# Optimization experiments

Measured on AMD Instinct MI355X. Metric: run time of the kernel, lower is better.

The kernel has to match this reference:

```python
import jax, jax.numpy as jnp
import numpy as np

N_HEAD = 16


def setup_inputs() -> dict:
    key = jax.random.key(0)
    ks = jax.random.split(key, 6)
    B, T, H = 4, 2048, 1024
    inp = jax.random.normal(ks[0], (B, T, H), dtype=jnp.float32)
    # padding mask: valid prefix of random length in [T//2, T] per batch row
    lengths = jax.random.randint(ks[1], (B, 1), T // 2, T + 1)
    mask = jnp.arange(T)[None, :] < lengths  # (B, T) bool
    s = 0.02
    w_qkv = jax.random.normal(ks[2], (H, 3 * H), dtype=jnp.float32) * s
    b_qkv = jax.random.normal(ks[3], (3 * H,), dtype=jnp.float32) * s
    w_out = jax.random.normal(ks[4], (H, H), dtype=jnp.float32) * s
    b_out = jax.random.normal(ks[5], (H,), dtype=jnp.float32) * s
    return {"input": inp, "mask": mask, "w_qkv": w_qkv, "b_qkv": b_qkv,
            "w_out": w_out, "b_out": b_out}


def reference(input, mask, w_qkv, b_qkv, w_out, b_out):
    B, T, H = input.shape
    hd = H // N_HEAD
    qkv = input @ w_qkv + b_qkv                       # (B, T, 3H)
    q, k, v = jnp.split(qkv, 3, axis=-1)
    # (B, T, H) -> (B, nh, T, hd)
    q = q.reshape(B, T, N_HEAD, hd).transpose(0, 2, 1, 3)
    k = k.reshape(B, T, N_HEAD, hd).transpose(0, 2, 1, 3)
    v = v.reshape(B, T, N_HEAD, hd).transpose(0, 2, 1, 3)
    scores = jnp.einsum('bhqd,bhkd->bhqk', q, k) / jnp.sqrt(jnp.float32(hd))
    causal = jnp.tril(jnp.ones((T, T), dtype=bool))   # (T, T)
    full_mask = causal[None, None, :, :] & mask[:, None, None, :]  # (B,1,T,T) bcast over heads
    scores = jnp.where(full_mask, scores, -jnp.inf)
    attn = jax.nn.softmax(scores, axis=-1)            # (B, nh, T, T)
    o = jnp.einsum('bhqk,bhkd->bhqd', attn, v)        # (B, nh, T, hd)
    o = o.transpose(0, 2, 1, 3).reshape(B, T, H)
    return o @ w_out + b_out
```

## Files before the change

### kernel.cpp

```cpp
#include <hip/hip_runtime.h>
#include <math.h>

#define B_  4
#define T_  2048
#define H_  1024
#define NH  16
#define HD  64
#define H3  3072

typedef short bf16x8 __attribute__((ext_vector_type(8)));
typedef short bf16x4 __attribute__((ext_vector_type(4)));
typedef float f32x4  __attribute__((ext_vector_type(4)));

#define SC2F 0.18033688011112042f

__device__ __forceinline__ unsigned short f2bf(float f) {
    union { float f; unsigned u; } v; v.f = f;
    unsigned u = v.u;
    unsigned r = (u + 0x7fffu + ((u >> 16) & 1u)) >> 16;
    return (unsigned short)r;
}

__device__ __forceinline__ void gload_lds16(const void* g, void* l) {
    __builtin_amdgcn_global_load_lds(
        (const __attribute__((address_space(1))) unsigned*)g,
        (__attribute__((address_space(3))) unsigned*)l, 16, 0, 0);
}

__device__ __forceinline__ f32x4 mfma_16x16x16_bf16(bf16x4 a, bf16x4 b, f32x4 c) {
#if __has_builtin(__builtin_amdgcn_mfma_f32_16x16x16_bf16)
    return __builtin_amdgcn_mfma_f32_16x16x16_bf16(a, b, c, 0, 0, 0);
#elif __has_builtin(__builtin_amdgcn_mfma_f32_16x16x16bf16_1k)
    return __builtin_amdgcn_mfma_f32_16x16x16bf16_1k(a, b, c, 0, 0, 0);
#else
    f32x4 d;
    asm volatile("v_mfma_f32_16x16x16_bf16 %0, %1, %2, %3"
                 : "=v"(d) : "v"(a), "v"(b), "v"(c));
    return d;
#endif
}

__global__ void lengths_kernel(const void* mask, int* lengths) {
    int b = blockIdx.x;
    int t = threadIdx.x;
    const unsigned* mu = (const unsigned*)mask;
    bool is_byte = (mu[0] == 0x01010101u);
    int cnt = 0;
    if (is_byte) {
        const unsigned char* m8 = (const unsigned char*)mask;
        for (int i = t; i < T_; i += 256) cnt += (m8[b * T_ + i] != 0);
    } else {
        const unsigned* m32 = (const unsigned*)mask;
        for (int i = t; i < T_; i += 256) cnt += (m32[b * T_ + i] != 0);
    }
    __shared__ int red[256];
    red[t] = cnt;
    __syncthreads();
    for (int s = 128; s > 0; s >>= 1) {
        if (t < s) red[t] += red[t + s];
        __syncthreads();
    }
    if (t == 0) lengths[b] = red[0];
}

__global__ void convert_bf16_kernel(const float* __restrict__ x,
                                    unsigned short* __restrict__ y, int n) {
    int i = (blockIdx.x * 256 + threadIdx.x) * 4;
    if (i < n) {
        float4 v = *(const float4*)(x + i);
        ushort4 o;
        o.x = f2bf(v.x); o.y = f2bf(v.y); o.z = f2bf(v.z); o.w = f2bf(v.w);
        *(ushort4*)(y + i) = o;
    }
}

__global__ void transpose_bf16_kernel(const float* __restrict__ in,
                                      unsigned short* __restrict__ out,
                                      int K, int N) {
    __shared__ unsigned short tile[32][33];
    int kb = blockIdx.y * 32, nb = blockIdx.x * 32;
    int tx = threadIdx.x, ty = threadIdx.y;
    for (int i = 0; i < 32; i += 8)
        tile[ty + i][tx] = f2bf(in[(long)(kb + ty + i) * N + nb + tx]);
    __syncthreads();
    for (int i = 0; i < 32; i += 8)
        out[(long)(nb + ty + i) * K + kb + tx] = tile[tx][ty + i];
}

template <bool BF16_OUT, bool KSCALE, bool VSPLIT>
__global__ __launch_bounds__(256) void gemm_kernel(
    const unsigned short* __restrict__ A,
    const unsigned short* __restrict__ Bt,
    const float* __restrict__ bias,
    void* __restrict__ C,
    unsigned short* __restrict__ Vt,
    int M, int N, int K)
{
    __shared__ unsigned short Asm[128][32];
    __shared__ unsigned short Bsm[128][32];

    int tn = blockIdx.x * 128, tm = blockIdx.y * 128;
    int tid = threadIdx.x;
    int wid = tid >> 6, lane = tid & 63, quad = lane >> 4, lr = lane & 15;
    int wm = (wid & 1) * 64, wn = (wid >> 1) * 64;
    int grow = lane >> 2, gcol = (lane & 3) * 8;

    f32x4 acc[4][4] = {};

    for (int k0 = 0; k0 < K; k0 += 32) {
        __syncthreads();
#pragma unroll
        for (int t = 0; t < 2; t++) {
            int ar = wid * 32 + t * 16 + grow;
            gload_lds16(A  + (long)(tm + ar) * K + k0 + gcol, &Asm[wid * 32 + t * 16][0]);
            gload_lds16(Bt + (long)(tn + ar) * K + k0 + gcol, &Bsm[wid * 32 + t * 16][0]);
        }
        __syncthreads();

        bf16x8 af[4], bfv[4];
#pragma unroll
        for (int i = 0; i < 4; i++) af[i]  = *(const bf16x8*)(&Asm[wm + i * 16 + lr][quad * 8]);
#pragma unroll
        for (int j = 0; j < 4; j++) bfv[j] = *(const bf16x8*)(&Bsm[wn + j * 16 + lr][quad * 8]);
#pragma unroll
        for (int i = 0; i < 4; i++)
#pragma unroll
            for (int j = 0; j < 4; j++)
                acc[i][j] = __builtin_amdgcn_mfma_f32_16x16x32_bf16(af[i], bfv[j], acc[i][j], 0, 0, 0);
    }

    if (VSPLIT && tn >= 2 * H_) {
#pragma unroll
        for (int i = 0; i < 4; i++)
#pragma unroll
            for (int j = 0; j < 4; j++) {
                int col = tn + wn + j * 16 + lr;
                float bs = bias[col];
                int feat = col - 2 * H_;
                int tok0 = tm + wm + i * 16 + quad * 4;
                int bb = tok0 >> 11;
                unsigned d0 = (unsigned)f2bf(acc[i][j][0] + bs) |
                              ((unsigned)f2bf(acc[i][j][1] + bs) << 16);
                unsigned d1 = (unsigned)f2bf(acc[i][j][2] + bs) |
                              ((unsigned)f2bf(acc[i][j][3] + bs) << 16);
                unsigned short* dst = Vt + ((long)(bb * 1024 + feat)) * T_ + (tok0 & (T_ - 1));
                *(uint2*)dst = make_uint2(d0, d1);
            }
        return;
    }

#pragma unroll
    for (int i = 0; i < 4; i++)
#pragma unroll
        for (int j = 0; j < 4; j++) {
            int col = tn + wn + j * 16 + lr;
            float bs = bias[col];
            bool ks = KSCALE && (col >= H_) && (col < 2 * H_);
#pragma unroll
            for (int r = 0; r < 4; r++) {
                int row = tm + wm + i * 16 + quad * 4 + r;
                float v = acc[i][j][r] + bs;
                if (ks) v *= SC2F;
                if (BF16_OUT)
                    ((unsigned short*)C)[(long)row * N + col] = f2bf(v);
                else
                    ((float*)C)[(long)row * N + col] = v;
            }
        }
}

__global__ __launch_bounds__(256) void attn_kernel(
    const unsigned short* __restrict__ QKV,
    const unsigned short* __restrict__ Vt,
    const int* __restrict__ lengths,
    unsigned short* __restrict__ O)
{
    int idx = blockIdx.x;
    int bh = idx & 63;
    int pr = idx >> 6;
    int b = bh >> 4, h = bh & 15;
    int len = lengths[b];

    int tid = threadIdx.x;
    int wid = tid >> 6, lane = tid & 63, quad = lane >> 4, lr = lane & 15;

    __shared__ unsigned short Qs[128][72];
    __shared__ unsigned short Kd[2][64][72];
    __shared__ unsigned short Vd[2][64][72];

    const long qkv_base = (long)b * T_ * H3;
    int srow = tid >> 2, scb = (tid & 3) * 16;
    const unsigned short* kbase = QKV + qkv_base + (long)srow * H3 + H_ + h * HD + scb;
    const unsigned short* vbase = Vt + ((long)(bh * 64 + srow)) * T_ + scb;

    for (int pass = 0; pass < 2; pass++) {
        int qt = pass ? pr : (15 - pr);
        int q0 = qt * 128;

        __syncthreads();
        {
            int row = tid >> 1, cb = (tid & 1) * 32;
            const unsigned short* src = QKV + qkv_base + (long)(q0 + row) * H3 + h * HD + cb;
#pragma unroll
            for (int i = 0; i < 4; i++)
                *(float4*)(&Qs[row][cb + i * 8]) = *(const float4*)(src + i * 8);
        }
        {
            float4 k0 = *(const float4*)(kbase);
            float4 k1 = *(const float4*)(kbase + 8);
            float4 v0 = *(const float4*)(vbase);
            float4 v1 = *(const float4*)(vbase + 8);
            *(float4*)(&Kd[0][srow][scb])     = k0;
            *(float4*)(&Kd[0][srow][scb + 8]) = k1;
            *(float4*)(&Vd[0][srow][scb])     = v0;
            *(float4*)(&Vd[0][srow][scb + 8]) = v1;
        }
        __syncthreads();

        bf16x8 qf[2][2];
#pragma unroll
        for (int nq = 0; nq < 2; nq++)
#pragma unroll
            for (int ks = 0; ks < 2; ks++)
                qf[nq][ks] = *(const bf16x8*)(&Qs[wid * 32 + nq * 16 + lr][ks * 32 + quad * 8]);

        float l_i[2] = { 0.f, 0.f };
        f32x4 Oacc[4][2] = {};

        int kmax = min(q0 + 127, len - 1);
        int n_kt = (kmax >> 6) + 1;
        int q_wave_lo = q0 + wid * 32;
        int q_wave_hi = q_wave_lo + 31;
        int myq[2] = { q_wave_lo + lr, q_wave_lo + 16 + lr };

        const unsigned short* kp = kbase + (long)64 * H3;
        const unsigned short* vp = vbase + 64;

        for (int kt = 0; kt < n_kt; kt++) {
            int cur = kt & 1;
            float4 pk0, pk1, pv0, pv1;
            bool pf = (kt + 1 < n_kt);
            if (pf) {
                pk0 = *(const float4*)(kp);
                pk1 = *(const float4*)(kp + 8);
                pv0 = *(const float4*)(vp);
                pv1 = *(const float4*)(vp + 8);
                kp += (long)64 * H3;
                vp += 64;
            }

            int k_lo = kt * 64;
            if (!(k_lo > q_wave_hi || k_lo >= len)) {
                f32x4 Sacc[4][2] = {};
#pragma unroll
                for (int ks = 0; ks < 2; ks++) {
#pragma unroll
                    for (int mt = 0; mt < 4; mt++) {
                        bf16x8 kf = *(const bf16x8*)(&Kd[cur][mt * 16 + lr][ks * 32 + quad * 8]);
                        Sacc[mt][0] = __builtin_amdgcn_mfma_f32_16x16x32_bf16(kf, qf[0][ks], Sacc[mt][0], 0, 0, 0);
                        Sacc[mt][1] = __builtin_amdgcn_mfma_f32_16x16x32_bf16(kf, qf[1][ks], Sacc[mt][1], 0, 0, 0);
                    }
                }

                bool full = (k_lo + 63 <= q_wave_lo) && (k_lo + 63 < len);
                float rs[2] = { 0.f, 0.f };
                unsigned pkk[4][2][2];
#pragma unroll
                for (int mt = 0; mt < 4; mt++)
#pragma unroll
                    for (int nq = 0; nq < 2; nq++) {
                        float p[4];
#pragma unroll
                        for (int r = 0; r < 4; r++) {
                            float s = Sacc[mt][nq][r];
                            if (!full) {
                                int key = k_lo + mt * 16 + quad * 4 + r;
                                bool ok = (key <= myq[nq]) && (key < len);
                                s = ok ? s : -INFINITY;
                            }
                            p[r] = __builtin_amdgcn_exp2f(s);
                            rs[nq] += p[r];
                        }
                        pkk[mt][nq][0] = __builtin_amdgcn_perm(__float_as_uint(p[1]), __float_as_uint(p[0]), 0x07060302);
                        pkk[mt][nq][1] = __builtin_amdgcn_perm(__float_as_uint(p[3]), __float_as_uint(p[2]), 0x07060302);
                    }

#pragma unroll
                for (int nq = 0; nq < 2; nq++) {
                    float v = rs[nq];
                    v += __shfl_xor(v, 16);
                    v += __shfl_xor(v, 32);
                    l_i[nq] += v;
                }

#pragma unroll
                for (int mt = 0; mt < 4; mt++) {
                    union { unsigned u[2]; bf16x4 v; } bu[2];
                    bu[0].u[0] = pkk[mt][0][0]; bu[0].u[1] = pkk[mt][0][1];
                    bu[1].u[0] = pkk[mt][1][0]; bu[1].u[1] = pkk[mt][1][1];
#pragma unroll
                    for (int md = 0; md < 4; md++) {
                        bf16x4 vf = *(const bf16x4*)(&Vd[cur][md * 16 + lr][mt * 16 + quad * 4]);
                        Oacc[md][0] = mfma_16x16x16_bf16(vf, bu[0].v, Oacc[md][0]);
                        Oacc[md][1] = mfma_16x16x16_bf16(vf, bu[1].v, Oacc[md][1]);
                    }
                }
            }

            if (pf) {
                *(float4*)(&Kd[cur ^ 1][srow][scb])     = pk0;
                *(float4*)(&Kd[cur ^ 1][srow][scb + 8]) = pk1;
                *(float4*)(&Vd[cur ^ 1][srow][scb])     = pv0;
                *(float4*)(&Vd[cur ^ 1][srow][scb + 8]) = pv1;
            }
            __syncthreads();
        }

        {
            float inv[2] = { 1.f / l_i[0], 1.f / l_i[1] };
#pragma unroll
            for (int nq = 0; nq < 2; nq++)
#pragma unroll
                for (int md = 0; md < 4; md++)
#pragma unroll
                    for (int rp = 0; rp < 2; rp++) {
                        float e0 = Oacc[md][nq][rp * 2]     * inv[nq];
                        float e1 = Oacc[md][nq][rp * 2 + 1] * inv[nq];
                        unsigned w = __builtin_amdgcn_perm(__float_as_uint(e1), __float_as_uint(e0), 0x07060302);
                        *(unsigned*)(&Qs[wid * 32 + nq * 16 + lr][md * 16 + quad * 4 + rp * 2]) = w;
                    }
            __asm__ volatile("s_waitcnt lgkmcnt(0)" ::: "memory");
            int row = lane >> 1, cb = (lane & 1) * 32;
            long tok = (long)b * T_ + q0 + wid * 32 + row;
#pragma unroll
            for (int i = 0; i < 4; i++) {
                float4 v = *(const float4*)(&Qs[wid * 32 + row][cb + i * 8]);
                *(float4*)(&O[tok * H_ + h * HD + cb + i * 8]) = v;
            }
        }
    }
}

extern "C" void kernel_launch(void* const* d_in, const int* in_sizes, int n_in,
                              void* d_out, int out_size, void* d_ws, size_t ws_size,
                              hipStream_t stream) {
    const float* X    = (const float*)d_in[0];
    const void*  mask = d_in[1];
    const float* Wqkv = (const float*)d_in[2];
    const float* bqkv = (const float*)d_in[3];
    const float* Wout = (const float*)d_in[4];
    const float* bout = (const float*)d_in[5];

    char* ws = (char*)d_ws;
    int* lengths          = (int*)ws;
    unsigned short* WqkvT = (unsigned short*)(ws + 256);
    unsigned short* WoutT = WqkvT + (long)H3 * H_;
    unsigned short* QKV   = WoutT + (long)H_ * H_;
    unsigned short* Xbf   = QKV + (long)B_ * T_ * H3;
    unsigned short* Vt    = Xbf + (long)B_ * T_ * H_;
    unsigned short* Obf   = Xbf;

    const int M = B_ * T_;

    lengths_kernel<<<B_, 256, 0, stream>>>(mask, lengths);
    convert_bf16_kernel<<<(M * H_ / 4 + 255) / 256, 256, 0, stream>>>(X, Xbf, M * H_);
    transpose_bf16_kernel<<<dim3(H3 / 32, H_ / 32), dim3(32, 8), 0, stream>>>(Wqkv, WqkvT, H_, H3);
    transpose_bf16_kernel<<<dim3(H_ / 32, H_ / 32), dim3(32, 8), 0, stream>>>(Wout, WoutT, H_, H_);
    gemm_kernel<true, true, true><<<dim3(H3 / 128, M / 128), 256, 0, stream>>>(
        Xbf, WqkvT, bqkv, QKV, Vt, M, H3, H_);
    attn_kernel<<<B_ * NH * 8, 256, 0, stream>>>(QKV, Vt, lengths, Obf);
    gemm_kernel<false, false, false><<<dim3(H_ / 128, M / 128), 256, 0, stream>>>(
        Obf, WoutT, bout, d_out, nullptr, M, H_, H_);
}
```

Measured before the change: 300.0 us.

## Drop LDS staging in attention, one q-tile per block; swizzle GEMM LDS

The attention kernel no longer stages K/V tiles in shared memory with double buffering and barriers. Each wave now loads its K and V fragments straight from global memory into registers and exits the key loop early per wave. The grid now launches one block per 128-query tile instead of pairing two tiles per block, so there are more blocks and no barriers in the main loop, at the cost of redundant global loads across waves and no causal load balancing within a block. Separately, the GEMM XOR-swizzles its LDS column layout to cut bank conflicts on fragment reads.

```diff
diff --git a/kernel.cpp b/kernel.cpp
--- a/kernel.cpp
+++ b/kernel.cpp
@@ -103,7 +103,9 @@
     int tid = threadIdx.x;
     int wid = tid >> 6, lane = tid & 63, quad = lane >> 4, lr = lane & 15;
     int wm = (wid & 1) * 64, wn = (wid >> 1) * 64;
-    int grow = lane >> 2, gcol = (lane & 3) * 8;
+    int grow = lane >> 2;
+    int gcol = (((lane & 3) ^ (grow & 3) ^ ((grow >> 2) & 3))) * 8;
+    int pc = ((quad ^ (lr & 3) ^ ((lr >> 2) & 3))) * 8;
 
     f32x4 acc[4][4] = {};
 
@@ -119,9 +121,9 @@
 
         bf16x8 af[4], bfv[4];
 #pragma unroll
-        for (int i = 0; i < 4; i++) af[i]  = *(const bf16x8*)(&Asm[wm + i * 16 + lr][quad * 8]);
-#pragma unroll
-        for (int j = 0; j < 4; j++) bfv[j] = *(const bf16x8*)(&Bsm[wn + j * 16 + lr][quad * 8]);
+        for (int i = 0; i < 4; i++) af[i]  = *(const bf16x8*)(&Asm[wm + i * 16 + lr][pc]);
+#pragma unroll
+        for (int j = 0; j < 4; j++) bfv[j] = *(const bf16x8*)(&Bsm[wn + j * 16 + lr][pc]);
 #pragma unroll
         for (int i = 0; i < 4; i++)
 #pragma unroll
@@ -177,166 +179,129 @@
 {
     int idx = blockIdx.x;
     int bh = idx & 63;
-    int pr = idx >> 6;
+    int qt = 15 - (idx >> 6);
     int b = bh >> 4, h = bh & 15;
     int len = lengths[b];
+    int q0 = qt * 128;
 
     int tid = threadIdx.x;
     int wid = tid >> 6, lane = tid & 63, quad = lane >> 4, lr = lane & 15;
 
-    __shared__ unsigned short Qs[128][72];
-    __shared__ unsigned short Kd[2][64][72];
-    __shared__ unsigned short Vd[2][64][72];
+    __shared__ unsigned short Es[128][68];
 
     const long qkv_base = (long)b * T_ * H3;
-    int srow = tid >> 2, scb = (tid & 3) * 16;
-    const unsigned short* kbase = QKV + qkv_base + (long)srow * H3 + H_ + h * HD + scb;
-    const unsigned short* vbase = Vt + ((long)(bh * 64 + srow)) * T_ + scb;
-
-    for (int pass = 0; pass < 2; pass++) {
-        int qt = pass ? pr : (15 - pr);
-        int q0 = qt * 128;
-
-        __syncthreads();
-        {
-            int row = tid >> 1, cb = (tid & 1) * 32;
-            const unsigned short* src = QKV + qkv_base + (long)(q0 + row) * H3 + h * HD + cb;
-#pragma unroll
-            for (int i = 0; i < 4; i++)
-                *(float4*)(&Qs[row][cb + i * 8]) = *(const float4*)(src + i * 8);
-        }
-        {
-            float4 k0 = *(const float4*)(kbase);
-            float4 k1 = *(const float4*)(kbase + 8);
-            float4 v0 = *(const float4*)(vbase);
-            float4 v1 = *(const float4*)(vbase + 8);
-            *(float4*)(&Kd[0][srow][scb])     = k0;
-            *(float4*)(&Kd[0][srow][scb + 8]) = k1;
-            *(float4*)(&Vd[0][srow][scb])     = v0;
-            *(float4*)(&Vd[0][srow][scb + 8]) = v1;
-        }
-        __syncthreads();
-
-        bf16x8 qf[2][2];
+
+    bf16x8 qf[2][2];
+#pragma unroll
+    for (int nq = 0; nq < 2; nq++)
+#pragma unroll
+        for (int ks = 0; ks < 2; ks++)
+            qf[nq][ks] = *(const bf16x8*)(QKV + qkv_base +
+                (long)(q0 + wid * 32 + nq * 16 + lr) * H3 + h * HD + ks * 32 + quad * 8);
+
+    float l_i[2] = { 0.f, 0.f };
+    f32x4 Oacc[4][2] = {};
+
+    int kmax = min(q0 + 127, len - 1);
+    int n_kt = (kmax >> 6) + 1;
+    int q_wave_lo = q0 + wid * 32;
+    int q_wave_hi = q_wave_lo + 31;
+    int myq[2] = { q_wave_lo + lr, q_wave_lo + 16 + lr };
+
+    const unsigned short* kptr = QKV + qkv_base + (long)lr * H3 + H_ + h * HD + quad * 8;
+    const unsigned short* vptr = Vt + ((long)(bh * 64 + lr)) * T_ + quad * 4;
+
+    for (int kt = 0; kt < n_kt; kt++) {
+        int k_lo = kt * 64;
+        if (k_lo > q_wave_hi || k_lo >= len) break;
+
+        bf16x4 vf[4][4];
+#pragma unroll
+        for (int md = 0; md < 4; md++)
+#pragma unroll
+            for (int mt = 0; mt < 4; mt++)
+                vf[md][mt] = *(const bf16x4*)(vptr + (long)(md * 16) * T_ + k_lo + mt * 16);
+
+        bf16x8 kf[4][2];
+#pragma unroll
+        for (int mt = 0; mt < 4; mt++)
+#pragma unroll
+            for (int ks = 0; ks < 2; ks++)
+                kf[mt][ks] = *(const bf16x8*)(kptr + (long)(k_lo + mt * 16) * H3 + ks * 32);
+
+        f32x4 Sacc[4][2] = {};
+#pragma unroll
+        for (int ks = 0; ks < 2; ks++)
+#pragma unroll
+            for (int mt = 0; mt < 4; mt++) {
+                Sacc[mt][0] = __builtin_amdgcn_mfma_f32_16x16x32_bf16(kf[mt][ks], qf[0][ks], Sacc[mt][0], 0, 0, 0);
+                Sacc[mt][1] = __builtin_amdgcn_mfma_f32_16x16x32_bf16(kf[mt][ks], qf[1][ks], Sacc[mt][1], 0, 0, 0);
+            }
+
+        bool full = (k_lo + 63 <= q_wave_lo) && (k_lo + 63 < len);
+        float rs[2] = { 0.f, 0.f };
+        unsigned pkk[4][2][2];
+#pragma unroll
+        for (int mt = 0; mt < 4; mt++)
+#pragma unroll
+            for (int nq = 0; nq < 2; nq++) {
+                float p[4];
+#pragma unroll
+                for (int r = 0; r < 4; r++) {
+                    float s = Sacc[mt][nq][r];
+                    if (!full) {
+                        int key = k_lo + mt * 16 + quad * 4 + r;
+                        bool ok = (key <= myq[nq]) && (key < len);
+                        s = ok ? s : -INFINITY;
+                    }
+                    p[r] = __builtin_amdgcn_exp2f(s);
+                    rs[nq] += p[r];
+                }
+                pkk[mt][nq][0] = __builtin_amdgcn_perm(__float_as_uint(p[1]), __float_as_uint(p[0]), 0x07060302);
+                pkk[mt][nq][1] = __builtin_amdgcn_perm(__float_as_uint(p[3]), __float_as_uint(p[2]), 0x07060302);
+            }
+
+#pragma unroll
+        for (int nq = 0; nq < 2; nq++) {
+            float v = rs[nq];
+            v += __shfl_xor(v, 16);
+            v += __shfl_xor(v, 32);
+            l_i[nq] += v;
+        }
+
+#pragma unroll
+        for (int mt = 0; mt < 4; mt++) {
+            union { unsigned u[2]; bf16x4 v; } bu[2];
+            bu[0].u[0] = pkk[mt][0][0]; bu[0].u[1] = pkk[mt][0][1];
+            bu[1].u[0] = pkk[mt][1][0]; bu[1].u[1] = pkk[mt][1][1];
+#pragma unroll
+            for (int md = 0; md < 4; md++) {
+                Oacc[md][0] = mfma_16x16x16_bf16(vf[md][mt], bu[0].v, Oacc[md][0]);
+                Oacc[md][1] = mfma_16x16x16_bf16(vf[md][mt], bu[1].v, Oacc[md][1]);
+            }
+        }
+    }
+
+    {
+        float inv[2] = { 1.f / l_i[0], 1.f / l_i[1] };
 #pragma unroll
         for (int nq = 0; nq < 2; nq++)
 #pragma unroll
-            for (int ks = 0; ks < 2; ks++)
-                qf[nq][ks] = *(const bf16x8*)(&Qs[wid * 32 + nq * 16 + lr][ks * 32 + quad * 8]);
-
-        float l_i[2] = { 0.f, 0.f };
-        f32x4 Oacc[4][2] = {};
-
-        int kmax = min(q0 + 127, len - 1);
-        int n_kt = (kmax >> 6) + 1;
-        int q_wave_lo = q0 + wid * 32;
-        int q_wave_hi = q_wave_lo + 31;
-        int myq[2] = { q_wave_lo + lr, q_wave_lo + 16 + lr };
-
-        const unsigned short* kp = kbase + (long)64 * H3;
-        const unsigned short* vp = vbase + 64;
-
-        for (int kt = 0; kt < n_kt; kt++) {
-            int cur = kt & 1;
-            float4 pk0, pk1, pv0, pv1;
-            bool pf = (kt + 1 < n_kt);
-            if (pf) {
-                pk0 = *(const float4*)(kp);
-                pk1 = *(const float4*)(kp + 8);
-                pv0 = *(const float4*)(vp);
-                pv1 = *(const float4*)(vp + 8);
-                kp += (long)64 * H3;
-                vp += 64;
-            }
-
-            int k_lo = kt * 64;
-            if (!(k_lo > q_wave_hi || k_lo >= len)) {
-                f32x4 Sacc[4][2] = {};
-#pragma unroll
-                for (int ks = 0; ks < 2; ks++) {
-#pragma unroll
-                    for (int mt = 0; mt < 4; mt++) {
-                        bf16x8 kf = *(const bf16x8*)(&Kd[cur][mt * 16 + lr][ks * 32 + quad * 8]);
-                        Sacc[mt][0] = __builtin_amdgcn_mfma_f32_16x16x32_bf16(kf, qf[0][ks], Sacc[mt][0], 0, 0, 0);
-                        Sacc[mt][1] = __builtin_amdgcn_mfma_f32_16x16x32_bf16(kf, qf[1][ks], Sacc[mt][1], 0, 0, 0);
-                    }
+            for (int md = 0; md < 4; md++)
+#pragma unroll
+                for (int rp = 0; rp < 2; rp++) {
+                    float e0 = Oacc[md][nq][rp * 2]     * inv[nq];
+                    float e1 = Oacc[md][nq][rp * 2 + 1] * inv[nq];
+                    unsigned w = __builtin_amdgcn_perm(__float_as_uint(e1), __float_as_uint(e0), 0x07060302);
+                    *(unsigned*)(&Es[wid * 32 + nq * 16 + lr][md * 16 + quad * 4 + rp * 2]) = w;
                 }
-
-                bool full = (k_lo + 63 <= q_wave_lo) && (k_lo + 63 < len);
-                float rs[2] = { 0.f, 0.f };
-                unsigned pkk[4][2][2];
-#pragma unroll
-                for (int mt = 0; mt < 4; mt++)
-#pragma unroll
-                    for (int nq = 0; nq < 2; nq++) {
-                        float p[4];
-#pragma unroll
-                        for (int r = 0; r < 4; r++) {
-                            float s = Sacc[mt][nq][r];
-                            if (!full) {
-                                int key = k_lo + mt * 16 + quad * 4 + r;
-                                bool ok = (key <= myq[nq]) && (key < len);
-                                s = ok ? s : -INFINITY;
-                            }
-                            p[r] = __builtin_amdgcn_exp2f(s);
-                            rs[nq] += p[r];
-                        }
-                        pkk[mt][nq][0] = __builtin_amdgcn_perm(__float_as_uint(p[1]), __float_as_uint(p[0]), 0x07060302);
-                        pkk[mt][nq][1] = __builtin_amdgcn_perm(__float_as_uint(p[3]), __float_as_uint(p[2]), 0x07060302);
-                    }
-
-#pragma unroll
-                for (int nq = 0; nq < 2; nq++) {
-                    float v = rs[nq];
-                    v += __shfl_xor(v, 16);
-                    v += __shfl_xor(v, 32);
-                    l_i[nq] += v;
-                }
-
-#pragma unroll
-                for (int mt = 0; mt < 4; mt++) {
-                    union { unsigned u[2]; bf16x4 v; } bu[2];
-                    bu[0].u[0] = pkk[mt][0][0]; bu[0].u[1] = pkk[mt][0][1];
-                    bu[1].u[0] = pkk[mt][1][0]; bu[1].u[1] = pkk[mt][1][1];
-#pragma unroll
-                    for (int md = 0; md < 4; md++) {
-                        bf16x4 vf = *(const bf16x4*)(&Vd[cur][md * 16 + lr][mt * 16 + quad * 4]);
-                        Oacc[md][0] = mfma_16x16x16_bf16(vf, bu[0].v, Oacc[md][0]);
-                        Oacc[md][1] = mfma_16x16x16_bf16(vf, bu[1].v, Oacc[md][1]);
-                    }
-                }
-            }
-
-            if (pf) {
-                *(float4*)(&Kd[cur ^ 1][srow][scb])     = pk0;
-                *(float4*)(&Kd[cur ^ 1][srow][scb + 8]) = pk1;
-                *(float4*)(&Vd[cur ^ 1][srow][scb])     = pv0;
-                *(float4*)(&Vd[cur ^ 1][srow][scb + 8]) = pv1;
-            }
-            __syncthreads();
-        }
-
-        {
-            float inv[2] = { 1.f / l_i[0], 1.f / l_i[1] };
-#pragma unroll
-            for (int nq = 0; nq < 2; nq++)
-#pragma unroll
-                for (int md = 0; md < 4; md++)
-#pragma unroll
-                    for (int rp = 0; rp < 2; rp++) {
-                        float e0 = Oacc[md][nq][rp * 2]     * inv[nq];
-                        float e1 = Oacc[md][nq][rp * 2 + 1] * inv[nq];
-                        unsigned w = __builtin_amdgcn_perm(__float_as_uint(e1), __float_as_uint(e0), 0x07060302);
-                        *(unsigned*)(&Qs[wid * 32 + nq * 16 + lr][md * 16 + quad * 4 + rp * 2]) = w;
-                    }
-            __asm__ volatile("s_waitcnt lgkmcnt(0)" ::: "memory");
-            int row = lane >> 1, cb = (lane & 1) * 32;
-            long tok = (long)b * T_ + q0 + wid * 32 + row;
-#pragma unroll
-            for (int i = 0; i < 4; i++) {
-                float4 v = *(const float4*)(&Qs[wid * 32 + row][cb + i * 8]);
-                *(float4*)(&O[tok * H_ + h * HD + cb + i * 8]) = v;
-            }
+        __asm__ volatile("s_waitcnt lgkmcnt(0)" ::: "memory");
+        int row = lane >> 1, cb = (lane & 1) * 32;
+        long tok = (long)b * T_ + q0 + wid * 32 + row;
+#pragma unroll
+        for (int i = 0; i < 4; i++) {
+            float4 v = *(const float4*)(&Es[wid * 32 + row][cb + i * 8]);
+            *(float4*)(&O[tok * H_ + h * HD + cb + i * 8]) = v;
         }
     }
 }
@@ -368,7 +333,7 @@
     transpose_bf16_kernel<<<dim3(H_ / 32, H_ / 32), dim3(32, 8), 0, stream>>>(Wout, WoutT, H_, H_);
     gemm_kernel<true, true, true><<<dim3(H3 / 128, M / 128), 256, 0, stream>>>(
         Xbf, WqkvT, bqkv, QKV, Vt, M, H3, H_);
-    attn_kernel<<<B_ * NH * 8, 256, 0, stream>>>(QKV, Vt, lengths, Obf);
+    attn_kernel<<<B_ * NH * (T_ / 128), 256, 0, stream>>>(QKV, Vt, lengths, Obf);
     gemm_kernel<false, false, false><<<dim3(H_ / 128, M / 128), 256, 0, stream>>>(
         Obf, WoutT, bout, d_out, nullptr, M, H_, H_);
 }
```

Result: slower. 413.6 us (+37.9%).
